# Optimization experiments

Hardware: AMD Instinct MI355X
Metric: run time of the kernel (lower is better)

The kernel has to match this reference:

```python
import jax, jax.numpy as jnp
import numpy as np

D_MODEL = 512
N_HEADS = 8
D_HEAD = D_MODEL // N_HEADS


def setup_inputs() -> dict:
    key = jax.random.key(0)
    ks = jax.random.split(key, 11)
    B, S = 2, 4096
    scale = 1.0 / np.sqrt(D_MODEL)
    inp = {
        "q": jax.random.normal(ks[0], (B, S, D_MODEL), dtype=jnp.float32),
        "k": jax.random.normal(ks[1], (B, S, D_MODEL), dtype=jnp.float32),
        "v": jax.random.normal(ks[2], (B, S, D_MODEL), dtype=jnp.float32),
        "Wq": jax.random.normal(ks[3], (D_MODEL, D_MODEL), dtype=jnp.float32) * scale,
        "bq": jnp.zeros((D_MODEL,), dtype=jnp.float32),
        "Wk": jax.random.normal(ks[4], (D_MODEL, D_MODEL), dtype=jnp.float32) * scale,
        "bk": jnp.zeros((D_MODEL,), dtype=jnp.float32),
        "Wv": jax.random.normal(ks[5], (D_MODEL, D_MODEL), dtype=jnp.float32) * scale,
        "bv": jnpp if False else jnp.zeros((D_MODEL,), dtype=jnp.float32),
        "Wo": jax.random.normal(ks[6], (D_MODEL, D_MODEL), dtype=jnp.float32) * scale,
        "bo": jnp.zeros((D_MODEL,), dtype=jnp.float32),
    }
    return inp


def reference(q, k, v, Wq, bq, Wk, bk, Wv, bv, Wo, bo):
    B, S, _ = q.shape
    # Linear projections (torch Linear: x @ W^T + b), split into heads -> [B,H,S,Dh]
    def proj(x, W, b):
        y = jnp.einsum("bsd,ed->bse", x, W) + b
        return y.reshape(B, -1, N_HEADS, D_HEAD).transpose(0, 2, 1, 3)

    Q = proj(q, Wq, bq)
    K = proj(k, Wk, bk)
    V = proj(v, Wv, bv)

    inv_sqrt_dh = 1.0 / np.sqrt(D_HEAD).astype(np.float32)
    scores = jnp.einsum("bhqd,bhkd->bhqk", Q, K) * inv_sqrt_dh  # [B,H,S,S]
    attn = jax.nn.softmax(scores, axis=-1)  # dropout is identity at eval
    out = jnp.einsum("bhqk,bhkd->bhqd", attn, V)  # [B,H,S,Dh]
    out = out.transpose(0, 2, 1, 3).reshape(B, S, D_MODEL)
    return jnp.einsum("bsd,ed->bse", out, Wo) + bo
```

## Files before the change

kernel.cpp:

```cpp
#include <hip/hip_runtime.h>
#include <hip/hip_bf16.h>
#include <hip/hip_fp16.h>
#include <stdint.h>

#define D_MODEL 512
#define NH 8
#define DH 64
#define BB 2
#define SS 4096
#define MTOT (BB*SS)

typedef __attribute__((ext_vector_type(8))) short bf16x8;
typedef __attribute__((ext_vector_type(4))) float f32x4;
typedef __fp16 fp16x2 __attribute__((ext_vector_type(2)));

#define MFMA32(a,b,c) __builtin_amdgcn_mfma_f32_16x16x32_bf16(a,b,c,0,0,0)

#if __has_builtin(__builtin_amdgcn_exp2f)
  #define EXP2F(x) __builtin_amdgcn_exp2f(x)
#else
  #define EXP2F(x) __expf((x) * 0.6931471805599453f)
#endif

#define QSCALE 0.18033688011112042f
#define EXPOFF 11.541560327679939f

__device__ __forceinline__ unsigned f2b(float f) {
  return (__float_as_uint(f) + 0x8000u) >> 16;
}
__device__ __forceinline__ float h2f(unsigned short h) {
  return __half2float(__ushort_as_half(h));
}
__device__ __forceinline__ unsigned packh2(float lo, float hi) {
  fp16x2 h = __builtin_amdgcn_cvt_pkrtz(lo, hi);
  return __builtin_bit_cast(unsigned, h);
}
__device__ __forceinline__ unsigned packpair(float lo, float hi) {
  return __builtin_amdgcn_perm(__float_as_uint(hi) + 0x8000u,
                               __float_as_uint(lo) + 0x8000u, 0x07060302u);
}
__device__ __forceinline__ unsigned cvtpk_bf16(float lo, float hi) {
  unsigned r;
  asm("v_cvt_pk_bf16_f32 %0, %1, %2" : "=v"(r) : "v"(lo), "v"(hi));
  return r;
}
__device__ __forceinline__ void gload_lds16(const unsigned short* g, unsigned short* l) {
  __builtin_amdgcn_global_load_lds(
      (const __attribute__((address_space(1))) unsigned int*)g,
      (__attribute__((address_space(3))) unsigned int*)l, 16, 0, 0);
}

struct PrepArgs {
  const float* src[7];
  unsigned short* dst[7];
  int off[8];
};

__global__ __launch_bounds__(256) void prep_kernel(PrepArgs a) {
  const int bx = blockIdx.x;
  int tgt = 0;
#pragma unroll
  for (int s = 1; s < 7; s++) tgt += (bx >= a.off[s]);
  const int i = ((bx - a.off[tgt]) * 256 + threadIdx.x) * 4;
  const float4 f = *(const float4*)(a.src[tgt] + i);
  uint2 o;
  o.x = packpair(f.x, f.y);
  o.y = packpair(f.z, f.w);
  *(uint2*)(a.dst[tgt] + i) = o;
}

struct CombArgs {
  const unsigned short* Os[4];
  const float* ls[4];
  unsigned short* Ao;
};

__global__ __launch_bounds__(256) void combine_kernel(CombArgs c) {
  const size_t i = ((size_t)blockIdx.x * 256 + threadIdx.x) * 8;
  const int m = (int)(i >> 9);
  const int k = (int)(i & 511);
  const int hh = k >> 6;
  const float inv = __builtin_amdgcn_rcpf(
      c.ls[0][(size_t)m * NH + hh] + c.ls[1][(size_t)m * NH + hh] +
      c.ls[2][(size_t)m * NH + hh] + c.ls[3][(size_t)m * NH + hh]);
  float sum[8] = {0.f, 0.f, 0.f, 0.f, 0.f, 0.f, 0.f, 0.f};
#pragma unroll
  for (int s = 0; s < 4; s++) {
    uint4 hv = *(const uint4*)(c.Os[s] + i);
    const unsigned short* he = (const unsigned short*)&hv;
#pragma unroll
    for (int e = 0; e < 8; e++) sum[e] += h2f(he[e]);
  }
  uint4 pk;
  pk.x = packpair(sum[0] * inv, sum[1] * inv);
  pk.y = packpair(sum[2] * inv, sum[3] * inv);
  pk.z = packpair(sum[4] * inv, sum[5] * inv);
  pk.w = packpair(sum[6] * inv, sum[7] * inv);
  *(uint4*)(c.Ao + i) = pk;
}

struct GemmArgs {
  const unsigned short* A[3];
  const unsigned short* W[3];
  const float* bias[3];
  unsigned short* out[3];
  float* outf;
  int mode;
};

__global__ __launch_bounds__(256) void gemm_kernel(GemmArgs g) {
  const int z = blockIdx.z;
  const float* __restrict__ bias = g.bias[z];
  unsigned short* __restrict__ out = g.out[z];
  const bool vt = (g.mode == 0) && (z == 2);
  const float osc = (g.mode == 0 && z == 0) ? QSCALE : 1.0f;

  __shared__ __align__(128) unsigned short lA[128][32];
  __shared__ __align__(128) unsigned short lB[128][32];

  const int t = threadIdx.x;
  const int lane = t & 63;
  const int w = t >> 6;
  const int wr = w >> 1, wc = w & 1;
  const int lrow = lane & 15, quad = lane >> 4;
  const int m0 = blockIdx.y * 128;
  const int n0 = blockIdx.x * 128;

  const int srow = lane >> 2;
  const int schunk = (lane & 3) * 8;

  const unsigned short* __restrict__ Ag = g.A[z];
  const unsigned short* __restrict__ Wg = g.W[z];

  f32x4 acc[4][4];
  for (int i = 0; i < 4; i++)
    for (int j = 0; j < 4; j++)
      for (int r = 0; r < 4; r++) acc[i][j][r] = 0.f;

  for (int kk = 0; kk < 512; kk += 32) {
#pragma unroll
    for (int i = 0; i < 2; i++) {
      const int r0 = w * 32 + i * 16;
      gload_lds16(Ag + (size_t)(m0 + r0 + srow) * 512 + kk + schunk, &lA[r0][0]);
      gload_lds16(Wg + (size_t)(n0 + r0 + srow) * 512 + kk + schunk, &lB[r0][0]);
    }
    __syncthreads();
    bf16x8 af[4], bfr[4];
#pragma unroll
    for (int mt = 0; mt < 4; mt++) af[mt] = *(const bf16x8*)&lA[wr * 64 + mt * 16 + lrow][quad * 8];
#pragma unroll
    for (int nt = 0; nt < 4; nt++) bfr[nt] = *(const bf16x8*)&lB[wc * 64 + nt * 16 + lrow][quad * 8];
#pragma unroll
    for (int mt = 0; mt < 4; mt++)
#pragma unroll
      for (int nt = 0; nt < 4; nt++)
        acc[mt][nt] = MFMA32(af[mt], bfr[nt], acc[mt][nt]);
    __syncthreads();
  }

  float bv[4];
#pragma unroll
  for (int nt = 0; nt < 4; nt++) bv[nt] = bias[n0 + wc * 64 + nt * 16 + lrow];

#pragma unroll
  for (int mt = 0; mt < 4; mt++) {
#pragma unroll
    for (int nt = 0; nt < 4; nt++) {
      const int n = n0 + wc * 64 + nt * 16 + lrow;
      const int mB = m0 + wr * 64 + mt * 16 + quad * 4;
      float val[4];
#pragma unroll
      for (int r = 0; r < 4; r++) val[r] = (acc[mt][nt][r] + bv[nt]) * osc;

      if (g.mode == 1) {
#pragma unroll
        for (int r = 0; r < 4; r++) g.outf[(size_t)(mB + r) * 512 + n] = val[r];
      } else if (vt) {
        const int bb = mB >> 12, s = mB & 4095;
        const int a = s >> 2;
        const int c0 = (s & ~31) + (a & 4) + ((a & 3) << 3);
        const int hh = n >> 6, dh = n & 63;
        ushort4 pk = make_ushort4((unsigned short)f2b(val[0]), (unsigned short)f2b(val[1]),
                                  (unsigned short)f2b(val[2]), (unsigned short)f2b(val[3]));
        *(ushort4*)(out + (((size_t)bb * NH + hh) * DH + dh) * SS + c0) = pk;
      } else {
        const int bb = mB >> 12;
        const int hh = n >> 6, dh = n & 63;
#pragma unroll
        for (int r = 0; r < 4; r++) {
          const int s = (mB + r) & 4095;
          out[((((size_t)bb * NH + hh) * SS + s) << 6) + dh] = (unsigned short)f2b(val[r]);
        }
      }
    }
  }
}

struct AttnArgs {
  const unsigned short* Qh;
  const unsigned short* Kh;
  const unsigned short* Vt;
  unsigned short* Op[4];
  float* lp[4];
};

__global__ __launch_bounds__(512, 4) void attn_kernel(AttnArgs a) {
  __shared__ __align__(16) unsigned short lK[64][72];
  __shared__ __align__(16) unsigned short lV[64][72];

  const int t = threadIdx.x;
  const int lane = t & 63;
  const int w = t >> 6;
  const int lrow = lane & 15, quad = lane >> 4;
  const int h = blockIdx.y, b = blockIdx.z;
  const int qtile = blockIdx.x & 15, jq = blockIdx.x >> 4;
  const size_t kb = ((size_t)b * NH + h) * SS * DH;
  const size_t vb = ((size_t)b * NH + h) * DH * SS;
  const int qrow0 = qtile * 256 + w * 32;
  unsigned short* __restrict__ Op = a.Op[jq];
  float* __restrict__ lp = a.lp[jq];
  const int jt0 = jq * 16, jt1 = jt0 + 16;

  bf16x8 qf[2][2];
#pragma unroll
  for (int ti = 0; ti < 2; ti++) {
    const unsigned short* qp = a.Qh + kb + (size_t)(qrow0 + ti * 16 + lrow) * DH + quad * 8;
    qf[ti][0] = *(const bf16x8*)qp;
    qf[ti][1] = *(const bf16x8*)(qp + 32);
  }

  f32x4 o[2][4];
  float lsum[2] = {0.f, 0.f};
#pragma unroll
  for (int ti = 0; ti < 2; ti++)
    for (int nt = 0; nt < 4; nt++)
      for (int r = 0; r < 4; r++) o[ti][nt][r] = 0.f;

  const unsigned short* __restrict__ Kg = a.Kh + kb;
  const unsigned short* __restrict__ Vg = a.Vt + vb;

  const int rk = t >> 3;
  const int ck = (t & 7) * 8;

  uint4 kreg = *(const uint4*)(Kg + (size_t)(jt0 * 64 + rk) * DH + ck);
  uint4 vreg = *(const uint4*)(Vg + (size_t)rk * SS + jt0 * 64 + ck);

  const f32x4 sinit = {-EXPOFF, -EXPOFF, -EXPOFF, -EXPOFF};

  for (int jt = jt0; jt < jt1; jt++) {
    __syncthreads();
    *(uint4*)&lK[rk][ck] = kreg;
    *(uint4*)&lV[rk][ck] = vreg;
    {
      const int nb = (jt + 1 < jt1 ? jt + 1 : jt) * 64;
      kreg = *(const uint4*)(Kg + (size_t)(nb + rk) * DH + ck);
      vreg = *(const uint4*)(Vg + (size_t)rk * SS + nb + ck);
    }
    __syncthreads();

#pragma unroll
    for (int half = 0; half < 2; half++) {
      uint2 pw[2][2];
#pragma unroll
      for (int u = 0; u < 2; u++) {
        const int ntj = half * 2 + u;
        bf16x8 k0 = *(const bf16x8*)&lK[ntj * 16 + lrow][quad * 8];
        bf16x8 k1 = *(const bf16x8*)&lK[ntj * 16 + lrow][32 + quad * 8];
#pragma unroll
        for (int ti = 0; ti < 2; ti++) {
          f32x4 s = MFMA32(k0, qf[ti][0], sinit);
          s = MFMA32(k1, qf[ti][1], s);
          const float e0 = EXP2F(s[0]);
          const float e1 = EXP2F(s[1]);
          const float e2 = EXP2F(s[2]);
          const float e3 = EXP2F(s[3]);
          lsum[ti] += (e0 + e1) + (e2 + e3);
          pw[u][ti].x = cvtpk_bf16(e0, e1);
          pw[u][ti].y = cvtpk_bf16(e2, e3);
        }
      }
      bf16x8 pcat[2];
#pragma unroll
      for (int ti = 0; ti < 2; ti++) {
        uint4 c;
        c.x = pw[0][ti].x; c.y = pw[0][ti].y;
        c.z = pw[1][ti].x; c.w = pw[1][ti].y;
        pcat[ti] = __builtin_bit_cast(bf16x8, c);
      }
#pragma unroll
      for (int nt = 0; nt < 4; nt++) {
        bf16x8 vv = *(const bf16x8*)&lV[nt * 16 + lrow][half * 32 + quad * 8];
#pragma unroll
        for (int ti = 0; ti < 2; ti++)
          o[ti][nt] = MFMA32(vv, pcat[ti], o[ti][nt]);
      }
    }
  }

#pragma unroll
  for (int ti = 0; ti < 2; ti++) {
    float l = lsum[ti];
    l += __shfl_xor(l, 16);
    l += __shfl_xor(l, 32);
    const int si = qrow0 + ti * 16 + lrow;
    unsigned short* dst = Op + ((size_t)(b * SS + si)) * D_MODEL + h * DH;
#pragma unroll
    for (int nt = 0; nt < 4; nt++) {
      uint2 pk;
      pk.x = packh2(o[ti][nt][0], o[ti][nt][1]);
      pk.y = packh2(o[ti][nt][2], o[ti][nt][3]);
      *(uint2*)(dst + nt * 16 + quad * 4) = pk;
    }
    if (quad == 0)
      lp[(size_t)(b * SS + si) * NH + h] = l;
  }
}

extern "C" void kernel_launch(void* const* d_in, const int* in_sizes, int n_in,
                              void* d_out, int out_size, void* d_ws, size_t ws_size,
                              hipStream_t stream) {
  const float* q  = (const float*)d_in[0];
  const float* k  = (const float*)d_in[1];
  const float* v  = (const float*)d_in[2];
  const float* Wq = (const float*)d_in[3];
  const float* bq = (const float*)d_in[4];
  const float* Wk = (const float*)d_in[5];
  const float* bk = (const float*)d_in[6];
  const float* Wv = (const float*)d_in[7];
  const float* bv = (const float*)d_in[8];
  const float* Wo = (const float*)d_in[9];
  const float* bo = (const float*)d_in[10];

  const size_t NX = (size_t)MTOT * D_MODEL;
  const size_t NW = (size_t)D_MODEL * D_MODEL;

  char* p = (char*)d_ws;
  unsigned short* qb  = (unsigned short*)p; p += NX * 2;
  unsigned short* kbf = (unsigned short*)p; p += NX * 2;
  unsigned short* vbf = (unsigned short*)p; p += NX * 2;
  unsigned short* Wqb = (unsigned short*)p; p += NW * 2;
  unsigned short* Wkb = (unsigned short*)p; p += NW * 2;
  unsigned short* Wvb = (unsigned short*)p; p += NW * 2;
  unsigned short* Wob = (unsigned short*)p; p += NW * 2;
  unsigned short* Qh  = (unsigned short*)p; p += NX * 2;
  unsigned short* Kh  = (unsigned short*)p; p += NX * 2;
  unsigned short* Vtg = (unsigned short*)p; p += NX * 2;
  unsigned short* Ao  = (unsigned short*)p; p += NX * 2;
  unsigned short* Os[4];
  float* ls[4];
  for (int i = 0; i < 4; i++) { Os[i] = (unsigned short*)p; p += NX * 2; }
  for (int i = 0; i < 4; i++) { ls[i] = (float*)p; p += (size_t)MTOT * NH * 4; }

  PrepArgs pr;
  pr.src[0] = q;  pr.dst[0] = qb;
  pr.src[1] = k;  pr.dst[1] = kbf;
  pr.src[2] = v;  pr.dst[2] = vbf;
  pr.src[3] = Wq; pr.dst[3] = Wqb;
  pr.src[4] = Wk; pr.dst[4] = Wkb;
  pr.src[5] = Wv; pr.dst[5] = Wvb;
  pr.src[6] = Wo; pr.dst[6] = Wob;
  {
    const int nb[7] = {(int)(NX / 1024), (int)(NX / 1024), (int)(NX / 1024),
                       (int)(NW / 1024), (int)(NW / 1024), (int)(NW / 1024),
                       (int)(NW / 1024)};
    int acc = 0;
    for (int i = 0; i < 7; i++) { pr.off[i] = acc; acc += nb[i]; }
    pr.off[7] = acc;
    prep_kernel<<<dim3(acc, 1, 1), 256, 0, stream>>>(pr);
  }

  GemmArgs pa;
  pa.A[0] = qb; pa.A[1] = kbf; pa.A[2] = vbf;
  pa.W[0] = Wqb; pa.W[1] = Wkb; pa.W[2] = Wvb;
  pa.bias[0] = bq; pa.bias[1] = bk; pa.bias[2] = bv;
  pa.out[0] = Qh; pa.out[1] = Kh; pa.out[2] = Vtg;
  pa.outf = nullptr;
  pa.mode = 0;
  gemm_kernel<<<dim3(4, 64, 3), 256, 0, stream>>>(pa);

  AttnArgs aa;
  aa.Qh = Qh; aa.Kh = Kh; aa.Vt = Vtg;
  for (int i = 0; i < 4; i++) { aa.Op[i] = Os[i]; aa.lp[i] = ls[i]; }
  attn_kernel<<<dim3(64, NH, BB), 512, 0, stream>>>(aa);

  CombArgs ca;
  for (int i = 0; i < 4; i++) { ca.Os[i] = Os[i]; ca.ls[i] = ls[i]; }
  ca.Ao = Ao;
  combine_kernel<<<dim3((int)(NX / 8 / 256), 1, 1), 256, 0, stream>>>(ca);

  GemmArgs oa;
  oa.A[0] = Ao; oa.A[1] = Ao; oa.A[2] = Ao;
  oa.W[0] = Wob; oa.W[1] = Wob; oa.W[2] = Wob;
  oa.bias[0] = bo; oa.bias[1] = bo; oa.bias[2] = bo;
  oa.out[0] = nullptr; oa.out[1] = nullptr; oa.out[2] = nullptr;
  oa.outf = (float*)d_out;
  oa.mode = 1;
  gemm_kernel<<<dim3(4, 64, 1), 256, 0, stream>>>(oa);
}
```

Before: 227.5 us.

## Halve attention key split count and deepen GEMM K-tile to 64

The attention split-K factor drops from 4 to 2, so each block covers 32 key tiles and there are half as many partial outputs for the combine kernel to read. Separately, the projection GEMM now stages 64-wide K slices in LDS with two MFMA sub-steps per slice, halving the number of barrier pairs. The cost is fewer attention blocks (512 instead of 1024), which may reduce occupancy across CUs, and doubled GEMM LDS usage.

```diff
diff --git a/kernel.cpp b/kernel.cpp
--- a/kernel.cpp
+++ b/kernel.cpp
@@ -9,6 +9,7 @@
 #define BB 2
 #define SS 4096
 #define MTOT (BB*SS)
+#define NJQ 2
 
 typedef __attribute__((ext_vector_type(8))) short bf16x8;
 typedef __attribute__((ext_vector_type(4))) float f32x4;
@@ -70,8 +71,8 @@
 }
 
 struct CombArgs {
-  const unsigned short* Os[4];
-  const float* ls[4];
+  const unsigned short* Os[NJQ];
+  const float* ls[NJQ];
   unsigned short* Ao;
 };
 
@@ -80,12 +81,13 @@
   const int m = (int)(i >> 9);
   const int k = (int)(i & 511);
   const int hh = k >> 6;
-  const float inv = __builtin_amdgcn_rcpf(
-      c.ls[0][(size_t)m * NH + hh] + c.ls[1][(size_t)m * NH + hh] +
-      c.ls[2][(size_t)m * NH + hh] + c.ls[3][(size_t)m * NH + hh]);
+  float lsum = 0.f;
+#pragma unroll
+  for (int s = 0; s < NJQ; s++) lsum += c.ls[s][(size_t)m * NH + hh];
+  const float inv = __builtin_amdgcn_rcpf(lsum);
   float sum[8] = {0.f, 0.f, 0.f, 0.f, 0.f, 0.f, 0.f, 0.f};
 #pragma unroll
-  for (int s = 0; s < 4; s++) {
+  for (int s = 0; s < NJQ; s++) {
     uint4 hv = *(const uint4*)(c.Os[s] + i);
     const unsigned short* he = (const unsigned short*)&hv;
 #pragma unroll
@@ -115,8 +117,8 @@
   const bool vt = (g.mode == 0) && (z == 2);
   const float osc = (g.mode == 0 && z == 0) ? QSCALE : 1.0f;
 
-  __shared__ __align__(128) unsigned short lA[128][32];
-  __shared__ __align__(128) unsigned short lB[128][32];
+  __shared__ __align__(128) unsigned short lA[128][64];
+  __shared__ __align__(128) unsigned short lB[128][64];
 
   const int t = threadIdx.x;
   const int lane = t & 63;
@@ -126,8 +128,8 @@
   const int m0 = blockIdx.y * 128;
   const int n0 = blockIdx.x * 128;
 
-  const int srow = lane >> 2;
-  const int schunk = (lane & 3) * 8;
+  const int srow = lane >> 3;
+  const int schunk = (lane & 7) * 8;
 
   const unsigned short* __restrict__ Ag = g.A[z];
   const unsigned short* __restrict__ Wg = g.W[z];
@@ -137,24 +139,29 @@
     for (int j = 0; j < 4; j++)
       for (int r = 0; r < 4; r++) acc[i][j][r] = 0.f;
 
-  for (int kk = 0; kk < 512; kk += 32) {
-#pragma unroll
-    for (int i = 0; i < 2; i++) {
-      const int r0 = w * 32 + i * 16;
+  for (int kk = 0; kk < 512; kk += 64) {
+#pragma unroll
+    for (int i = 0; i < 4; i++) {
+      const int r0 = w * 32 + i * 8;
       gload_lds16(Ag + (size_t)(m0 + r0 + srow) * 512 + kk + schunk, &lA[r0][0]);
       gload_lds16(Wg + (size_t)(n0 + r0 + srow) * 512 + kk + schunk, &lB[r0][0]);
     }
     __syncthreads();
-    bf16x8 af[4], bfr[4];
-#pragma unroll
-    for (int mt = 0; mt < 4; mt++) af[mt] = *(const bf16x8*)&lA[wr * 64 + mt * 16 + lrow][quad * 8];
-#pragma unroll
-    for (int nt = 0; nt < 4; nt++) bfr[nt] = *(const bf16x8*)&lB[wc * 64 + nt * 16 + lrow][quad * 8];
-#pragma unroll
-    for (int mt = 0; mt < 4; mt++)
+#pragma unroll
+    for (int ks = 0; ks < 2; ks++) {
+      bf16x8 af[4], bfr[4];
+#pragma unroll
+      for (int mt = 0; mt < 4; mt++)
+        af[mt] = *(const bf16x8*)&lA[wr * 64 + mt * 16 + lrow][ks * 32 + quad * 8];
 #pragma unroll
       for (int nt = 0; nt < 4; nt++)
-        acc[mt][nt] = MFMA32(af[mt], bfr[nt], acc[mt][nt]);
+        bfr[nt] = *(const bf16x8*)&lB[wc * 64 + nt * 16 + lrow][ks * 32 + quad * 8];
+#pragma unroll
+      for (int mt = 0; mt < 4; mt++)
+#pragma unroll
+        for (int nt = 0; nt < 4; nt++)
+          acc[mt][nt] = MFMA32(af[mt], bfr[nt], acc[mt][nt]);
+    }
     __syncthreads();
   }
 
@@ -200,8 +207,8 @@
   const unsigned short* Qh;
   const unsigned short* Kh;
   const unsigned short* Vt;
-  unsigned short* Op[4];
-  float* lp[4];
+  unsigned short* Op[NJQ];
+  float* lp[NJQ];
 };
 
 __global__ __launch_bounds__(512, 4) void attn_kernel(AttnArgs a) {
@@ -219,7 +226,7 @@
   const int qrow0 = qtile * 256 + w * 32;
   unsigned short* __restrict__ Op = a.Op[jq];
   float* __restrict__ lp = a.lp[jq];
-  const int jt0 = jq * 16, jt1 = jt0 + 16;
+  const int jt0 = jq * 32, jt1 = jt0 + 32;
 
   bf16x8 qf[2][2];
 #pragma unroll
@@ -346,10 +353,10 @@
   unsigned short* Kh  = (unsigned short*)p; p += NX * 2;
   unsigned short* Vtg = (unsigned short*)p; p += NX * 2;
   unsigned short* Ao  = (unsigned short*)p; p += NX * 2;
-  unsigned short* Os[4];
-  float* ls[4];
-  for (int i = 0; i < 4; i++) { Os[i] = (unsigned short*)p; p += NX * 2; }
-  for (int i = 0; i < 4; i++) { ls[i] = (float*)p; p += (size_t)MTOT * NH * 4; }
+  unsigned short* Os[NJQ];
+  float* ls[NJQ];
+  for (int i = 0; i < NJQ; i++) { Os[i] = (unsigned short*)p; p += NX * 2; }
+  for (int i = 0; i < NJQ; i++) { ls[i] = (float*)p; p += (size_t)MTOT * NH * 4; }
 
   PrepArgs pr;
   pr.src[0] = q;  pr.dst[0] = qb;
@@ -380,11 +387,11 @@
 
   AttnArgs aa;
   aa.Qh = Qh; aa.Kh = Kh; aa.Vt = Vtg;
-  for (int i = 0; i < 4; i++) { aa.Op[i] = Os[i]; aa.lp[i] = ls[i]; }
-  attn_kernel<<<dim3(64, NH, BB), 512, 0, stream>>>(aa);
+  for (int i = 0; i < NJQ; i++) { aa.Op[i] = Os[i]; aa.lp[i] = ls[i]; }
+  attn_kernel<<<dim3(16 * NJQ, NH, BB), 512, 0, stream>>>(aa);
 
   CombArgs ca;
-  for (int i = 0; i < 4; i++) { ca.Os[i] = Os[i]; ca.ls[i] = ls[i]; }
+  for (int i = 0; i < NJQ; i++) { ca.Os[i] = Os[i]; ca.ls[i] = ls[i]; }
   ca.Ao = Ao;
   combine_kernel<<<dim3((int)(NX / 8 / 256), 1, 1), 256, 0, stream>>>(ca);
 
```

After: 234.0 us. +2.9%, slower.
